# Performance work log

Hardware: AMD Instinct MI355X
Metric: run time of the kernel (lower is better)

## Reference

```python
import jax, jax.numpy as jnp
import numpy as np
import math

B, T, D = 2, 2048, 1024
H, DH = 16, 64          # num_heads, head_dim
DFF = 4096              # 4*d_model
EPS = 1e-5


def _layernorm(x, g, b):
    m = jnp.mean(x, axis=-1, keepdims=True)
    v = jnp.mean(jnp.square(x - m), axis=-1, keepdims=True)
    return (x - m) * jax.lax.rsqrt(v + EPS) * g + b


def setup_inputs() -> dict:
    key = jax.random.key(0)
    ks = jax.random.split(key, 6)
    s = 0.02
    return {
        "x": jax.random.normal(ks[0], (B, T, D), dtype=jnp.float32),
        "ln1_g": jnp.ones((D,), jnp.float32), "ln1_b": jnp.zeros((D,), jnp.float32),
        "ln2_g": jnp.ones((D,), jnp.float32), "ln2_b": jnp.zeros((D,), jnp.float32),
        "w_qkv": jax.random.normal(ks[1], (3 * D, D), jnp.float32) * s,
        "b_qkv": jnp.zeros((3 * D,), jnp.float32),
        "w_out": jax.random.normal(ks[2], (D, D), jnp.float32) * s,
        "b_out": jnp.zeros((D,), jnp.float32),
        "w1": jax.random.normal(ks[3], (DFF, D), jnp.float32) * s,
        "b1": jnp.zeros((DFF,), jnp.float32),
        "w2": jax.random.normal(ks[4], (D, DFF), jnp.float32) * s,
        "b2": jnp.zeros((D,), jnp.float32),
    }


def reference(x, ln1_g, ln1_b, ln2_g, ln2_b, w_qkv, b_qkv, w_out, b_out, w1, b1, w2, b2):
    # --- attention sublayer (Pre-LN) ---
    h = _layernorm(x, ln1_g, ln1_b)                       # [B,T,D]
    qkv = h @ w_qkv.T + b_qkv                             # [B,T,3D]
    qkv = qkv.reshape(B, T, 3, H, DH).transpose(2, 0, 3, 1, 4)  # [3,B,H,T,DH]
    q, k, v = qkv[0], qkv[1], qkv[2]
    scores = jnp.einsum('bhqd,bhkd->bhqk', q, k) / math.sqrt(DH)  # [B,H,T,T]
    causal = jnp.tril(jnp.ones((T, T), dtype=bool))
    scores = jnp.where(causal, scores, -jnp.inf)
    weights = jax.nn.softmax(scores, axis=-1)
    attn = jnp.einsum('bhqk,bhkd->bhqd', weights, v)      # [B,H,T,DH]
    attn = attn.transpose(0, 2, 1, 3).reshape(B, T, D)
    x = x + (attn @ w_out.T + b_out)

    # --- FFN sublayer (Pre-LN, exact GELU) ---
    h2 = _layernorm(x, ln2_g, ln2_b)
    ff = jax.nn.gelu(h2 @ w1.T + b1, approximate=False) @ w2.T + b2
    return x + ff
```

## Files before the change

kernel.cpp:

```cpp
#include <hip/hip_runtime.h>
#include <hip/hip_bf16.h>
#include <cmath>

typedef __bf16 bf16x8 __attribute__((ext_vector_type(8)));
typedef float  f32x4  __attribute__((ext_vector_type(4)));

#define LDS_AS __attribute__((address_space(3)))
#define GLB_AS __attribute__((address_space(1)))

__device__ __forceinline__ void gll16(const void* g, void* l) {
    __builtin_amdgcn_global_load_lds((const GLB_AS unsigned int*)g,
                                     (LDS_AS unsigned int*)l, 16, 0, 0);
}

__device__ __forceinline__ f32x4 mfma16(bf16x8 a, bf16x8 b, f32x4 c) {
    return __builtin_amdgcn_mfma_f32_16x16x32_bf16(a, b, c, 0, 0, 0);
}

__device__ __forceinline__ unsigned short f2bf(float f) {
    __hip_bfloat16 b = __float2bfloat16(f);
    return *reinterpret_cast<unsigned short*>(&b);
}

__device__ __forceinline__ bf16x8 swzfrag(const __hip_bfloat16* __restrict__ lds,
                                          int row, int cb)
{
    const int addr = row * 128 + (cb ^ ((row & 7) << 4));
    return *(const bf16x8*)((const char*)lds + addr);
}

__device__ __forceinline__ void stage64x128B(const char* __restrict__ base, int pitch,
                                             char* __restrict__ lds, int t)
{
#pragma unroll
    for (int i = 0; i < 2; ++i) {
        const int d   = i * 4096 + t * 16;
        const int row = d >> 7;
        const int x   = d & 127;
        const int gx  = x ^ ((row & 7) << 4);
        gll16(base + (size_t)row * pitch + gx, lds + d);
    }
}

__device__ __forceinline__ void stage128x128B(const char* __restrict__ base, int pitch,
                                              char* __restrict__ lds, int t)
{
#pragma unroll
    for (int i = 0; i < 4; ++i) {
        const int d   = i * 4096 + t * 16;
        const int row = d >> 7;
        const int x   = d & 127;
        const int gx  = x ^ ((row & 7) << 4);
        gll16(base + (size_t)row * pitch + gx, lds + d);
    }
}

#define TB   2
#define TT   2048
#define TD   1024
#define TH   16
#define TDH  64
#define TDFF 4096
#define TM   4096

__global__ __launch_bounds__(256)
void cvt_kernel(const float* __restrict__ src, __hip_bfloat16* __restrict__ dst, int n4)
{
    int i = blockIdx.x * 256 + threadIdx.x;
    if (i >= n4) return;
    float4 v = ((const float4*)src)[i];
    ushort4 o;
    o.x = f2bf(v.x); o.y = f2bf(v.y); o.z = f2bf(v.z); o.w = f2bf(v.w);
    ((ushort4*)dst)[i] = o;
}

__global__ __launch_bounds__(256)
void ln_kernel(const float* __restrict__ x, const float* __restrict__ g,
               const float* __restrict__ b, __hip_bfloat16* __restrict__ out)
{
    const int row = blockIdx.x;
    const int t = threadIdx.x;
    const float4 v = *(const float4*)(x + (size_t)row * TD + t * 4);
    float s  = v.x + v.y + v.z + v.w;
    float ss = v.x*v.x + v.y*v.y + v.z*v.z + v.w*v.w;
#pragma unroll
    for (int d = 1; d < 64; d <<= 1) { s += __shfl_xor(s, d); ss += __shfl_xor(ss, d); }
    __shared__ float red[8];
    const int wv = t >> 6, lane = t & 63;
    if (lane == 0) { red[wv] = s; red[4 + wv] = ss; }
    __syncthreads();
    s  = red[0] + red[1] + red[2] + red[3];
    ss = red[4] + red[5] + red[6] + red[7];
    const float mean = s * (1.0f / TD);
    const float var  = ss * (1.0f / TD) - mean * mean;
    const float rstd = rsqrtf(var + 1e-5f);
    const float4 gv = *(const float4*)(g + t * 4);
    const float4 bv = *(const float4*)(b + t * 4);
    ushort4 o;
    o.x = f2bf((v.x - mean) * rstd * gv.x + bv.x);
    o.y = f2bf((v.y - mean) * rstd * gv.y + bv.y);
    o.z = f2bf((v.z - mean) * rstd * gv.z + bv.z);
    o.w = f2bf((v.w - mean) * rstd * gv.w + bv.w);
    *(ushort4*)(out + (size_t)row * TD + t * 4) = o;
}

template<int EPI>
__global__ __launch_bounds__(512)
void gemm_sk(const __hip_bfloat16* __restrict__ A, const __hip_bfloat16* __restrict__ Bw,
             const float* __restrict__ bias, const float* __restrict__ resid,
             float* __restrict__ outf, __hip_bfloat16* __restrict__ outb,
             __hip_bfloat16* __restrict__ qb, __hip_bfloat16* __restrict__ kb,
             __hip_bfloat16* __restrict__ vtb,
             int M, int N, int K)
{
    __shared__ char ldsraw[131072];
    const int t = threadIdx.x;
    const int tl = t & 255;
    const int lane = t & 63, w = t >> 6;
    const int grp = w >> 2;
    const int wl = w & 3;
    const int wr = wl >> 1, wc = wl & 1;
    const int l15 = lane & 15, lg = lane >> 4;
    const int bn = blockIdx.x, bm = blockIdx.y;

    f32x4 acc[4][4] = {};

    const int Kh = K >> 1;
    const char* Ab = (const char*)(A  + (size_t)bm * 128 * K) + (size_t)grp * Kh * 2;
    const char* Bb = (const char*)(Bw + (size_t)bn * 128 * K) + (size_t)grp * Kh * 2;
    const int pitch = K * 2;
    char* base = ldsraw + grp * 65536;

    const int nt = Kh >> 6;
    stage128x128B(Ab, pitch, base, tl);
    stage128x128B(Bb, pitch, base + 32768, tl);

    for (int it = 0; it < nt; ++it) {
        const int cb = (it & 1) * 16384;
        if (it + 1 < nt) {
            const size_t koff = (size_t)(it + 1) * 128;
            const int nb = ((it + 1) & 1) * 16384;
            stage128x128B(Ab + koff, pitch, base + nb, tl);
            stage128x128B(Bb + koff, pitch, base + 32768 + nb, tl);
            asm volatile("s_waitcnt vmcnt(8)" ::: "memory");
        } else {
            asm volatile("s_waitcnt vmcnt(0)" ::: "memory");
        }
        __builtin_amdgcn_s_barrier();
        __builtin_amdgcn_sched_barrier(0);
        const __hip_bfloat16* bufA = (const __hip_bfloat16*)(base + cb);
        const __hip_bfloat16* bufB = (const __hip_bfloat16*)(base + 32768 + cb);
        bf16x8 af[4][2], bfr[4][2];
#pragma unroll
        for (int mf = 0; mf < 4; ++mf)
#pragma unroll
            for (int kk = 0; kk < 2; ++kk)
                af[mf][kk] = swzfrag(bufA, wr * 64 + mf * 16 + l15, kk * 64 + lg * 16);
#pragma unroll
        for (int nf = 0; nf < 4; ++nf)
#pragma unroll
            for (int kk = 0; kk < 2; ++kk)
                bfr[nf][kk] = swzfrag(bufB, wc * 64 + nf * 16 + l15, kk * 64 + lg * 16);
        __builtin_amdgcn_s_setprio(1);
#pragma unroll
        for (int mf = 0; mf < 4; ++mf)
#pragma unroll
            for (int nf = 0; nf < 4; ++nf) {
                acc[mf][nf] = mfma16(af[mf][0], bfr[nf][0], acc[mf][nf]);
                acc[mf][nf] = mfma16(af[mf][1], bfr[nf][1], acc[mf][nf]);
            }
        __builtin_amdgcn_s_setprio(0);
        __builtin_amdgcn_s_barrier();
    }

    float* xch = (float*)ldsraw;
    if (grp == 1) {
#pragma unroll
        for (int mf = 0; mf < 4; ++mf)
#pragma unroll
            for (int nf = 0; nf < 4; ++nf)
#pragma unroll
                for (int r = 0; r < 4; ++r)
                    xch[(wr * 64 + mf * 16 + lg * 4 + r) * 132 + wc * 64 + nf * 16 + l15] =
                        acc[mf][nf][r];
    }
    __syncthreads();
    if (grp == 0) {
#pragma unroll
        for (int mf = 0; mf < 4; ++mf)
#pragma unroll
            for (int nf = 0; nf < 4; ++nf)
#pragma unroll
                for (int r = 0; r < 4; ++r) {
                    const int mgl = wr * 64 + mf * 16 + lg * 4 + r;
                    const int ngl = wc * 64 + nf * 16 + l15;
                    const int mg = bm * 128 + mgl;
                    const int ng = bn * 128 + ngl;
                    const float v = acc[mf][nf][r] + xch[mgl * 132 + ngl] + bias[ng];
                    if constexpr (EPI == 1) {
                        const size_t o = (size_t)mg * N + ng;
                        outf[o] = v + resid[o];
                    } else if constexpr (EPI == 2) {
                        const float ge = 0.5f * v * (1.0f + erff(v * 0.70710678118654752f));
                        outb[(size_t)mg * N + ng] = __float2bfloat16(ge);
                    } else {
                        const int which = ng >> 10;
                        const int hh = (ng >> 6) & 15;
                        const int dh = ng & 63;
                        const int bb = mg >> 11;
                        const int tt = mg & 2047;
                        const int bhid = bb * TH + hh;
                        const __hip_bfloat16 bv = __float2bfloat16(v);
                        if (which == 0)      qb[((size_t)bhid * TT + tt) * TDH + dh] = bv;
                        else if (which == 1) kb[((size_t)bhid * TT + tt) * TDH + dh] = bv;
                        else                 vtb[((size_t)bhid * TDH + dh) * TT + tt] = bv;
                    }
                }
    }
}

__global__ __launch_bounds__(256)
void flash_kernel(const __hip_bfloat16* __restrict__ q, const __hip_bfloat16* __restrict__ k,
                  const __hip_bfloat16* __restrict__ vt, __hip_bfloat16* __restrict__ attn)
{
    const int L  = blockIdx.y * gridDim.x + blockIdx.x;
    const int cu = L & 255;
    const int s  = L >> 8;
    const int q0 = cu & 31;
    const int qt = (s & 1) ? (31 - q0) : q0;
    const int bh = s * 8 + (cu >> 5);

    const int t = threadIdx.x;
    const int w = t >> 6, lane = t & 63;
    const int l15 = lane & 15, lg = lane >> 4;
    const int qrow0 = qt * 64 + w * 16;
    const __hip_bfloat16* Qb = q  + (size_t)bh * TT * TDH;
    const __hip_bfloat16* Kb = k  + (size_t)bh * TT * TDH;
    const __hip_bfloat16* Vb = vt + (size_t)bh * TDH * TT;

    __shared__ __hip_bfloat16 kt[2][64 * 64];
    __shared__ __hip_bfloat16 vtt[2][64 * 64];
    __shared__ __hip_bfloat16 plds[4][16 * 64];

    bf16x8 qa[2];
#pragma unroll
    for (int c = 0; c < 2; ++c)
        qa[c] = *(const bf16x8*)(Qb + (size_t)(qrow0 + l15) * TDH + c * 32 + lg * 8);

    f32x4 o[4] = {};
    float mrun = -INFINITY, lrun = 0.0f;

    const int nt = qt + 1;
    int cur = 0;
    stage64x128B((const char*)Kb, 128, (char*)kt[0], t);
    stage64x128B((const char*)Vb, TT * 2, (char*)vtt[0], t);
    __syncthreads();

    for (int it = 0; it < nt; ++it) {
        const int kv0 = it * 64;
        if (it + 1 < nt) {
            stage64x128B((const char*)Kb + (size_t)(kv0 + 64) * 128, 128, (char*)kt[cur ^ 1], t);
            stage64x128B((const char*)Vb + (size_t)(kv0 + 64) * 2, TT * 2, (char*)vtt[cur ^ 1], t);
        }
        f32x4 sc[4] = {};
#pragma unroll
        for (int j = 0; j < 4; ++j) {
            const bf16x8 kb0 = swzfrag(kt[cur], j * 16 + l15, lg * 16);
            const bf16x8 kb1 = swzfrag(kt[cur], j * 16 + l15, 64 + lg * 16);
            sc[j] = mfma16(kb0, qa[0], sc[j]);
            sc[j] = mfma16(kb1, qa[1], sc[j]);
        }
        if (it == nt - 1) {
            const int qg = qrow0 + l15;
#pragma unroll
            for (int j = 0; j < 4; ++j)
#pragma unroll
                for (int r = 0; r < 4; ++r) {
                    const int kvg = kv0 + j * 16 + lg * 4 + r;
                    sc[j][r] = (kvg <= qg) ? sc[j][r] * 0.125f : -INFINITY;
                }
        } else {
#pragma unroll
            for (int j = 0; j < 4; ++j)
#pragma unroll
                for (int r = 0; r < 4; ++r) sc[j][r] *= 0.125f;
        }
        float pm;
        {
            float m0 = fmaxf(fmaxf(sc[0][0], sc[0][1]), fmaxf(sc[0][2], sc[0][3]));
            float m1 = fmaxf(fmaxf(sc[1][0], sc[1][1]), fmaxf(sc[1][2], sc[1][3]));
            float m2 = fmaxf(fmaxf(sc[2][0], sc[2][1]), fmaxf(sc[2][2], sc[2][3]));
            float m3 = fmaxf(fmaxf(sc[3][0], sc[3][1]), fmaxf(sc[3][2], sc[3][3]));
            pm = fmaxf(fmaxf(m0, m1), fmaxf(m2, m3));
        }
        pm = fmaxf(pm, __shfl_xor(pm, 16));
        pm = fmaxf(pm, __shfl_xor(pm, 32));

        const float mn = fmaxf(mrun, pm);
        const float alpha = __expf(mrun - mn);
        mrun = mn;
        f32x4 p[4];
        float rs = 0.0f;
#pragma unroll
        for (int j = 0; j < 4; ++j) {
            float a = 0.0f;
#pragma unroll
            for (int r = 0; r < 4; ++r) { p[j][r] = __expf(sc[j][r] - mn); a += p[j][r]; }
            rs += a;
        }
        rs += __shfl_xor(rs, 16);
        rs += __shfl_xor(rs, 32);
        lrun = lrun * alpha + rs;
#pragma unroll
        for (int nf = 0; nf < 4; ++nf)
#pragma unroll
            for (int r = 0; r < 4; ++r) o[nf][r] *= alpha;
        {
            __hip_bfloat16* pw = plds[w];
#pragma unroll
            for (int j = 0; j < 4; ++j) {
                ushort4 pk;
                pk.x = f2bf(p[j][0]); pk.y = f2bf(p[j][1]);
                pk.z = f2bf(p[j][2]); pk.w = f2bf(p[j][3]);
                const int cb = j * 32 + lg * 8;
                *(ushort4*)((char*)pw + l15 * 128 + (cb ^ ((l15 & 7) << 4))) = pk;
            }
        }
        asm volatile("s_waitcnt lgkmcnt(0)" ::: "memory");
        __builtin_amdgcn_sched_barrier(0);
        bf16x8 pb[2];
#pragma unroll
        for (int c = 0; c < 2; ++c)
            pb[c] = swzfrag(plds[w], l15, c * 64 + lg * 16);
#pragma unroll
        for (int nf = 0; nf < 4; ++nf) {
            const bf16x8 vb0 = swzfrag(vtt[cur], nf * 16 + l15, lg * 16);
            const bf16x8 vb1 = swzfrag(vtt[cur], nf * 16 + l15, 64 + lg * 16);
            o[nf] = mfma16(vb0, pb[0], o[nf]);
            o[nf] = mfma16(vb1, pb[1], o[nf]);
        }
        __syncthreads();
        cur ^= 1;
    }

    const int bb = bh >> 4, hh = bh & 15;
    const float inv = 1.0f / lrun;
    const int tt = qrow0 + l15;
#pragma unroll
    for (int nf = 0; nf < 4; ++nf) {
        const int d0 = nf * 16 + lg * 4;
        ushort4 st;
        st.x = f2bf(o[nf][0] * inv);
        st.y = f2bf(o[nf][1] * inv);
        st.z = f2bf(o[nf][2] * inv);
        st.w = f2bf(o[nf][3] * inv);
        *(ushort4*)(attn + ((size_t)(bb * TT + tt)) * TD + hh * TDH + d0) = st;
    }
}

extern "C" void kernel_launch(void* const* d_in, const int* in_sizes, int n_in,
                              void* d_out, int out_size, void* d_ws, size_t ws_size,
                              hipStream_t stream)
{
    const float* x     = (const float*)d_in[0];
    const float* ln1_g = (const float*)d_in[1];
    const float* ln1_b = (const float*)d_in[2];
    const float* ln2_g = (const float*)d_in[3];
    const float* ln2_b = (const float*)d_in[4];
    const float* w_qkv = (const float*)d_in[5];
    const float* b_qkv = (const float*)d_in[6];
    const float* w_out = (const float*)d_in[7];
    const float* b_out = (const float*)d_in[8];
    const float* w1    = (const float*)d_in[9];
    const float* b1    = (const float*)d_in[10];
    const float* w2    = (const float*)d_in[11];
    const float* b2    = (const float*)d_in[12];

    char* ws = (char*)d_ws;
    __hip_bfloat16* wqkv_bf = (__hip_bfloat16*)(ws + 0);
    __hip_bfloat16* wout_bf = (__hip_bfloat16*)(ws + 6291456);
    __hip_bfloat16* w1_bf   = (__hip_bfloat16*)(ws + 8388608);
    __hip_bfloat16* w2_bf   = (__hip_bfloat16*)(ws + 16777216);
    float*          x2      = (float*)(ws + 25165824);
    __hip_bfloat16* hbuf    = (__hip_bfloat16*)(ws + 41943040);
    __hip_bfloat16* qbuf    = (__hip_bfloat16*)(ws + 50331648);
    __hip_bfloat16* kbuf    = (__hip_bfloat16*)(ws + 58720256);
    __hip_bfloat16* vtbuf   = (__hip_bfloat16*)(ws + 67108864);
    __hip_bfloat16* attnbuf = (__hip_bfloat16*)(ws + 75497472);
    __hip_bfloat16* ff1     = (__hip_bfloat16*)(ws + 50331648);

    cvt_kernel<<<3072, 256, 0, stream>>>(w_qkv, wqkv_bf, 3 * TD * TD / 4);
    cvt_kernel<<<1024, 256, 0, stream>>>(w_out, wout_bf, TD * TD / 4);
    cvt_kernel<<<4096, 256, 0, stream>>>(w1, w1_bf, TDFF * TD / 4);
    cvt_kernel<<<4096, 256, 0, stream>>>(w2, w2_bf, TD * TDFF / 4);

    ln_kernel<<<TM, 256, 0, stream>>>(x, ln1_g, ln1_b, hbuf);
    gemm_sk<0><<<dim3(24, 32), 512, 0, stream>>>(hbuf, wqkv_bf, b_qkv, nullptr,
                                                 nullptr, nullptr, qbuf, kbuf, vtbuf,
                                                 TM, 3 * TD, TD);
    flash_kernel<<<dim3(32, 32), 256, 0, stream>>>(qbuf, kbuf, vtbuf, attnbuf);
    gemm_sk<1><<<dim3(8, 32), 512, 0, stream>>>(attnbuf, wout_bf, b_out, x,
                                                x2, nullptr, nullptr, nullptr, nullptr,
                                                TM, TD, TD);
    ln_kernel<<<TM, 256, 0, stream>>>(x2, ln2_g, ln2_b, hbuf);
    gemm_sk<2><<<dim3(32, 32), 512, 0, stream>>>(hbuf, w1_bf, b1, nullptr,
                                                 nullptr, ff1, nullptr, nullptr, nullptr,
                                                 TM, TDFF, TD);
    gemm_sk<1><<<dim3(8, 32), 512, 0, stream>>>(ff1, w2_bf, b2, x2,
                                                (float*)d_out, nullptr, nullptr, nullptr, nullptr,
                                                TM, TD, TDFF);
}
```

Measured before the change: 280.4 us.

## Add 256x256-tile pipelined GEMM for QKV and FFN1 projections

Introduces a new gemm256 kernel with 256x256 output tiles, 8 waves, double-buffered LDS staging interleaved across MFMA phases, explicit waitcnt/barrier scheduling and setprio around MFMA bursts. It replaces the split-K 128x128 gemm_sk for the QKV and W1 projections. Larger tiles give more data reuse per byte loaded and drop the split-K reduction through LDS. The cost is fewer blocks: 192 and 256 blocks on a 256-CU part, so the QKV launch leaves some CUs idle. The larger register footprint may also lower occupancy.

```diff
diff --git a/kernel.cpp b/kernel.cpp
--- a/kernel.cpp
+++ b/kernel.cpp
@@ -48,6 +48,19 @@
 #pragma unroll
     for (int i = 0; i < 4; ++i) {
         const int d   = i * 4096 + t * 16;
+        const int row = d >> 7;
+        const int x   = d & 127;
+        const int gx  = x ^ ((row & 7) << 4);
+        gll16(base + (size_t)row * pitch + gx, lds + d);
+    }
+}
+
+__device__ __forceinline__ void stage128x128B_512(const char* __restrict__ base, int pitch,
+                                                  char* __restrict__ lds, int t)
+{
+#pragma unroll
+    for (int i = 0; i < 2; ++i) {
+        const int d   = i * 8192 + t * 16;
         const int row = d >> 7;
         const int x   = d & 127;
         const int gx  = x ^ ((row & 7) << 4);
@@ -106,6 +119,144 @@
 
 template<int EPI>
 __global__ __launch_bounds__(512)
+void gemm256(const __hip_bfloat16* __restrict__ A, const __hip_bfloat16* __restrict__ Bw,
+             const float* __restrict__ bias,
+             __hip_bfloat16* __restrict__ outb,
+             __hip_bfloat16* __restrict__ qb, __hip_bfloat16* __restrict__ kb,
+             __hip_bfloat16* __restrict__ vtb,
+             int M, int N, int K)
+{
+    __shared__ __hip_bfloat16 ldsA[2][256 * 64];
+    __shared__ __hip_bfloat16 ldsB[2][256 * 64];
+    const int t = threadIdx.x;
+    const int lane = t & 63, w = t >> 6;
+    const int wm = w >> 2, wn = w & 3;
+    const int l15 = lane & 15, lg = lane >> 4;
+    const int bn = blockIdx.x, bm = blockIdx.y;
+
+    f32x4 acc[8][4] = {};
+    const char* Ab = (const char*)(A  + (size_t)bm * 256 * K);
+    const char* Bb = (const char*)(Bw + (size_t)bn * 256 * K);
+    const int pitch = K * 2;
+    const int nt = K >> 6;
+    const int niter = nt >> 1;
+
+    stage128x128B_512(Ab,                       pitch, (char*)ldsA[0],         t);
+    stage128x128B_512(Ab + (size_t)128 * pitch, pitch, (char*)ldsA[0] + 16384, t);
+    stage128x128B_512(Bb,                       pitch, (char*)ldsB[0],         t);
+    stage128x128B_512(Bb + (size_t)128 * pitch, pitch, (char*)ldsB[0] + 16384, t);
+    stage128x128B_512(Ab + 128,                 pitch, (char*)ldsA[1],         t);
+    asm volatile("s_waitcnt vmcnt(2)" ::: "memory");
+    __builtin_amdgcn_s_barrier();
+    __builtin_amdgcn_sched_barrier(0);
+
+    bf16x8 ar[4][2], br[4][2];
+
+    for (int i = 0; i < niter; ++i) {
+        const int t0 = 2 * i;
+        constexpr int STILE[8] = {1, 1, 1, 2, 2, 2, 2, 3};
+        constexpr int SPART[8] = {1, 2, 3, 0, 1, 2, 3, 0};
+#pragma unroll
+        for (int g = 0; g < 8; ++g) {
+            const int tt  = g >> 2;
+            const int p   = g & 3;
+            const int mfb = (p >> 1) * 4;
+            const int nfb = (p & 1) * 2;
+            const __hip_bfloat16* bufA = ldsA[tt];
+            const __hip_bfloat16* bufB = ldsB[tt];
+            if (p == 0) {
+#pragma unroll
+                for (int j = 0; j < 4; ++j) {
+                    ar[j][0] = swzfrag(bufA, wm * 128 + j * 16 + l15, lg * 16);
+                    ar[j][1] = swzfrag(bufA, wm * 128 + j * 16 + l15, 64 + lg * 16);
+                }
+#pragma unroll
+                for (int n = 0; n < 2; ++n) {
+                    br[n][0] = swzfrag(bufB, wn * 64 + n * 16 + l15, lg * 16);
+                    br[n][1] = swzfrag(bufB, wn * 64 + n * 16 + l15, 64 + lg * 16);
+                }
+            } else if (p == 1) {
+#pragma unroll
+                for (int n = 2; n < 4; ++n) {
+                    br[n][0] = swzfrag(bufB, wn * 64 + n * 16 + l15, lg * 16);
+                    br[n][1] = swzfrag(bufB, wn * 64 + n * 16 + l15, 64 + lg * 16);
+                }
+            } else if (p == 2) {
+#pragma unroll
+                for (int j = 0; j < 4; ++j) {
+                    ar[j][0] = swzfrag(bufA, wm * 128 + (4 + j) * 16 + l15, lg * 16);
+                    ar[j][1] = swzfrag(bufA, wm * 128 + (4 + j) * 16 + l15, 64 + lg * 16);
+                }
+            }
+            {
+                const int st = t0 + STILE[g];
+                if (st < nt) {
+                    char* dstA = (char*)ldsA[STILE[g] & 1];
+                    char* dstB = (char*)ldsB[STILE[g] & 1];
+                    if (SPART[g] == 0)
+                        stage128x128B_512(Ab + (size_t)st * 128, pitch, dstA, t);
+                    else if (SPART[g] == 1)
+                        stage128x128B_512(Ab + (size_t)128 * pitch + (size_t)st * 128, pitch, dstA + 16384, t);
+                    else if (SPART[g] == 2)
+                        stage128x128B_512(Bb + (size_t)st * 128, pitch, dstB, t);
+                    else
+                        stage128x128B_512(Bb + (size_t)128 * pitch + (size_t)st * 128, pitch, dstB + 16384, t);
+                }
+            }
+            if (p == 0) asm volatile("s_waitcnt lgkmcnt(8)" ::: "memory");
+            if (g == 3) {
+                if (t0 + 2 < nt) asm volatile("s_waitcnt vmcnt(2)" ::: "memory");
+                else             asm volatile("s_waitcnt vmcnt(0)" ::: "memory");
+            } else if (g == 7) {
+                if (t0 + 3 < nt) asm volatile("s_waitcnt vmcnt(2)" ::: "memory");
+            }
+            __builtin_amdgcn_s_barrier();
+            asm volatile("s_waitcnt lgkmcnt(0)" ::: "memory");
+            __builtin_amdgcn_sched_barrier(0);
+            __builtin_amdgcn_s_setprio(1);
+#pragma unroll
+            for (int j = 0; j < 4; ++j)
+#pragma unroll
+                for (int n = 0; n < 2; ++n) {
+                    acc[mfb + j][nfb + n] = mfma16(ar[j][0], br[nfb + n][0], acc[mfb + j][nfb + n]);
+                    acc[mfb + j][nfb + n] = mfma16(ar[j][1], br[nfb + n][1], acc[mfb + j][nfb + n]);
+                }
+            __builtin_amdgcn_s_setprio(0);
+            __builtin_amdgcn_s_barrier();
+        }
+    }
+
+#pragma unroll
+    for (int mf = 0; mf < 8; ++mf) {
+#pragma unroll
+        for (int nf = 0; nf < 4; ++nf) {
+#pragma unroll
+            for (int r = 0; r < 4; ++r) {
+                const int mg = bm * 256 + wm * 128 + mf * 16 + lg * 4 + r;
+                const int ng = bn * 256 + wn * 64 + nf * 16 + l15;
+                const float v = acc[mf][nf][r] + bias[ng];
+                if constexpr (EPI == 2) {
+                    const float ge = 0.5f * v * (1.0f + erff(v * 0.70710678118654752f));
+                    outb[(size_t)mg * N + ng] = __float2bfloat16(ge);
+                } else {
+                    const int which = ng >> 10;
+                    const int hh = (ng >> 6) & 15;
+                    const int dh = ng & 63;
+                    const int bb = mg >> 11;
+                    const int tt2 = mg & 2047;
+                    const int bhid = bb * TH + hh;
+                    const __hip_bfloat16 bv = __float2bfloat16(v);
+                    if (which == 0)      qb[((size_t)bhid * TT + tt2) * TDH + dh] = bv;
+                    else if (which == 1) kb[((size_t)bhid * TT + tt2) * TDH + dh] = bv;
+                    else                 vtb[((size_t)bhid * TDH + dh) * TT + tt2] = bv;
+                }
+            }
+        }
+    }
+}
+
+template<int EPI>
+__global__ __launch_bounds__(512)
 void gemm_sk(const __hip_bfloat16* __restrict__ A, const __hip_bfloat16* __restrict__ Bw,
              const float* __restrict__ bias, const float* __restrict__ resid,
              float* __restrict__ outf, __hip_bfloat16* __restrict__ outb,
@@ -200,20 +351,6 @@
                     if constexpr (EPI == 1) {
                         const size_t o = (size_t)mg * N + ng;
                         outf[o] = v + resid[o];
-                    } else if constexpr (EPI == 2) {
-                        const float ge = 0.5f * v * (1.0f + erff(v * 0.70710678118654752f));
-                        outb[(size_t)mg * N + ng] = __float2bfloat16(ge);
-                    } else {
-                        const int which = ng >> 10;
-                        const int hh = (ng >> 6) & 15;
-                        const int dh = ng & 63;
-                        const int bb = mg >> 11;
-                        const int tt = mg & 2047;
-                        const int bhid = bb * TH + hh;
-                        const __hip_bfloat16 bv = __float2bfloat16(v);
-                        if (which == 0)      qb[((size_t)bhid * TT + tt) * TDH + dh] = bv;
-                        else if (which == 1) kb[((size_t)bhid * TT + tt) * TDH + dh] = bv;
-                        else                 vtb[((size_t)bhid * TDH + dh) * TT + tt] = bv;
                     }
                 }
     }
@@ -395,16 +532,16 @@
     cvt_kernel<<<4096, 256, 0, stream>>>(w2, w2_bf, TD * TDFF / 4);
 
     ln_kernel<<<TM, 256, 0, stream>>>(x, ln1_g, ln1_b, hbuf);
-    gemm_sk<0><<<dim3(24, 32), 512, 0, stream>>>(hbuf, wqkv_bf, b_qkv, nullptr,
-                                                 nullptr, nullptr, qbuf, kbuf, vtbuf,
+    gemm256<0><<<dim3(12, 16), 512, 0, stream>>>(hbuf, wqkv_bf, b_qkv,
+                                                 nullptr, qbuf, kbuf, vtbuf,
                                                  TM, 3 * TD, TD);
     flash_kernel<<<dim3(32, 32), 256, 0, stream>>>(qbuf, kbuf, vtbuf, attnbuf);
     gemm_sk<1><<<dim3(8, 32), 512, 0, stream>>>(attnbuf, wout_bf, b_out, x,
                                                 x2, nullptr, nullptr, nullptr, nullptr,
                                                 TM, TD, TD);
     ln_kernel<<<TM, 256, 0, stream>>>(x2, ln2_g, ln2_b, hbuf);
-    gemm_sk<2><<<dim3(32, 32), 512, 0, stream>>>(hbuf, w1_bf, b1, nullptr,
-                                                 nullptr, ff1, nullptr, nullptr, nullptr,
+    gemm256<2><<<dim3(16, 16), 512, 0, stream>>>(hbuf, w1_bf, b1,
+                                                 ff1, nullptr, nullptr, nullptr,
                                                  TM, TDFF, TD);
     gemm_sk<1><<<dim3(8, 32), 512, 0, stream>>>(ff1, w2_bf, b2, x2,
                                                 (float*)d_out, nullptr, nullptr, nullptr, nullptr,
```

After: 288.9 us. 3.0% more time.
